# Kernel optimization log

Hardware: AMD Instinct MI355X
Metric: run time of the kernel (lower is better)

Reference implementation:

```python
import jax, jax.numpy as jnp
import numpy as np

B, D, N, WD, R, NW = 1024, 1024, 256, 64, 4, 1
EPS = 1e-6


def _dense(x, W, b):
    return x @ W + b


def _cosine_weights(memory, keys, strengths):
    # memory [B,N,WD], keys [B,K,WD], strengths [B,K] -> softmax cosine weights [B,K,N]
    dot = jnp.einsum('bkw,bnw->bkn', keys, memory)
    mn = jnp.linalg.norm(memory, axis=-1)  # [B,N]
    kn = jnp.linalg.norm(keys, axis=-1)    # [B,K]
    sim = dot / (kn[:, :, None] * mn[:, None, :] + EPS)
    return jax.nn.softmax(sim * strengths[:, :, None], axis=-1)


def _allocation(usage):
    # DNC Freeness allocation: sort by non-usage, exclusive cumprod of usage, unsort.
    usage = EPS + (1.0 - EPS) * usage
    nonusage = 1.0 - usage
    idx = jnp.argsort(-nonusage, axis=-1)            # descending non-usage
    s_non = jnp.take_along_axis(nonusage, idx, axis=-1)
    s_use = 1.0 - s_non
    cp = jnp.cumprod(s_use, axis=-1)
    excl = jnp.concatenate([jnp.ones_like(cp[:, :1]), cp[:, :-1]], axis=-1)
    s_alloc = s_non * excl
    inv = jnp.argsort(idx, axis=-1)                  # inverse permutation
    return jnp.take_along_axis(s_alloc, inv, axis=-1)


def _forward(controller, memory, prev_read_weights, prev_write_weights, prev_link,
             prev_precedence, prev_usage, params):
    (W_wv, b_wv, W_ev, b_ev, W_fg, b_fg, W_ag, b_ag, W_wg, b_wg,
     W_rm, b_rm, W_ws, b_ws, W_rs, b_rs, W_wk, b_wk, W_rk, b_rk) = params
    Bsz = controller.shape[0]

    # _read_inputs: small dense projections of controller output
    write_vectors = _dense(controller, W_wv, b_wv).reshape(Bsz, NW, WD)
    erase_vectors = jax.nn.sigmoid(_dense(controller, W_ev, b_ev)).reshape(Bsz, NW, WD)
    free_gate = jax.nn.sigmoid(_dense(controller, W_fg, b_fg))          # [B,R]
    allocation_gate = jax.nn.sigmoid(_dense(controller, W_ag, b_ag))    # [B,NW]
    write_gate = jax.nn.sigmoid(_dense(controller, W_wg, b_wg))         # [B,NW]
    read_mode = jax.nn.softmax(_dense(controller, W_rm, b_rm).reshape(Bsz, R, 1 + 2 * NW), axis=-1)
    write_keys = _dense(controller, W_wk, b_wk).reshape(Bsz, NW, WD)
    write_strengths = jax.nn.softplus(_dense(controller, W_ws, b_ws))   # [B,NW]
    read_keys = _dense(controller, W_rk, b_rk).reshape(Bsz, R, WD)
    read_strengths = jax.nn.softplus(_dense(controller, W_rs, b_rs))    # [B,R]

    # Freeness: usage update (not differentiable wrt write weights, per DNC)
    ww_sg = jax.lax.stop_gradient(prev_write_weights)
    agg_ww = 1.0 - jnp.prod(1.0 - ww_sg, axis=1)                        # [B,N]
    usage_after_write = prev_usage + (1.0 - prev_usage) * agg_ww
    phi = jnp.prod(1.0 - free_gate[:, :, None] * prev_read_weights, axis=1)
    usage = usage_after_write * phi

    # write weights: content + allocation mixed by gates
    write_content = _cosine_weights(memory, write_keys, write_strengths)  # [B,NW,N]
    write_gates = allocation_gate * write_gate
    alloc_list = []
    u = usage
    for i in range(NW):
        a = _allocation(u)
        alloc_list.append(a)
        u = u + (1.0 - u) * write_gates[:, i:i + 1] * a
    write_alloc = jnp.stack(alloc_list, axis=1)                           # [B,NW,N]
    ag = allocation_gate[:, :, None]
    wg = write_gate[:, :, None]
    write_weights = wg * (ag * write_alloc + (1.0 - ag) * write_content)

    # erase and write
    weighted_resets = write_weights[:, :, :, None] * erase_vectors[:, :, None, :]  # [B,NW,N,WD]
    reset_gate = jnp.prod(1.0 - weighted_resets, axis=1)                           # [B,N,WD]
    memory = memory * reset_gate + jnp.einsum('bwn,bwd->bnd', write_weights, write_vectors)

    # temporal linkage update
    ww_i = write_weights[:, :, :, None]
    ww_j = write_weights[:, :, None, :]
    new_link = ww_i * prev_precedence[:, :, None, :]
    link = (1.0 - ww_i - ww_j) * prev_link + new_link
    link = link * (1.0 - jnp.eye(N, dtype=link.dtype))                   # zero diagonal
    precedence = (1.0 - jnp.sum(write_weights, axis=-1, keepdims=True)) * prev_precedence + write_weights

    # read weights: content + directional (forward/backward over link)
    read_content = _cosine_weights(memory, read_keys, read_strengths)    # [B,R,N]
    forward_w = jnp.einsum('brn,bwmn->brwm', prev_read_weights, link)    # adjoint_b=True
    backward_w = jnp.einsum('brn,bwnm->brwm', prev_read_weights, link)
    backward_mode = read_mode[:, :, :NW]
    forward_mode = read_mode[:, :, NW:2 * NW]
    content_mode = read_mode[:, :, 2 * NW]
    read_weights = (content_mode[:, :, None] * read_content
                    + jnp.einsum('brw,brwn->brn', forward_mode, forward_w)
                    + jnp.einsum('brw,brwn->brn', backward_mode, backward_w))
    read_words = jnp.einsum('brn,bnd->brd', read_weights, memory)        # [B,R,WD]
    return read_words, memory, read_weights, write_weights, link, precedence, usage


def setup_inputs() -> dict:
    key = jax.random.key(0)
    ks = jax.random.split(key, 32)
    inp = {
        'controller': jax.random.normal(ks[0], (B, D), jnp.float32),
        'memory': jax.random.normal(ks[1], (B, N, WD), jnp.float32),
        'prev_read_weights': jax.random.uniform(ks[2], (B, R, N), jnp.float32) / N,
        'prev_write_weights': jax.random.uniform(ks[3], (B, NW, N), jnp.float32) / N,
        'prev_link': jnp.zeros((B, NW, N, N), jnp.float32),
        'prev_precedence': jax.random.uniform(ks[4], (B, NW, N), jnp.float32) / N,
        'prev_usage': jax.random.uniform(ks[5], (B, N), jnp.float32),
    }
    dims = [('wv', NW * WD), ('ev', NW * WD), ('fg', R), ('ag', NW), ('wg', NW),
            ('rm', R * (1 + 2 * NW)), ('ws', NW), ('rs', R), ('wk', NW * WD), ('rk', R * WD)]
    i = 6
    for name, od in dims:
        inp['W_' + name] = jax.random.normal(ks[i], (D, od), jnp.float32) * 0.02
        inp['b_' + name] = jnp.zeros((od,), jnp.float32)
        i += 1
    return inp


def reference(controller, memory, prev_read_weights, prev_write_weights, prev_link,
              prev_precedence, prev_usage,
              W_wv, b_wv, W_ev, b_ev, W_fg, b_fg, W_ag, b_ag, W_wg, b_wg,
              W_rm, b_rm, W_ws, b_ws, W_rs, b_rs, W_wk, b_wk, W_rk, b_rk):
    params = (W_wv, b_wv, W_ev, b_ev, W_fg, b_fg, W_ag, b_ag, W_wg, b_wg,
              W_rm, b_rm, W_ws, b_ws, W_rs, b_rs, W_wk, b_wk, W_rk, b_rk)
    return _forward(controller, memory, prev_read_weights, prev_write_weights,
                    prev_link, prev_precedence, prev_usage, params)
```

## Files before the change

kernel.cpp:

```cpp
#include <hip/hip_runtime.h>
#include <math.h>

typedef unsigned short ush;
typedef float v4f __attribute__((ext_vector_type(4)));

#define EPSc 1e-6f

#define NB 1024
#define ND 1024
#define NN 256
#define NWD 64
#define NR 4

#define OFF_RWORDS   ((size_t)0)
#define OFF_MEM      ((size_t)262144)
#define OFF_RWEIGHTS ((size_t)17039360)
#define OFF_WW       ((size_t)18087936)
#define OFF_LINK     ((size_t)18350080)
#define OFF_PREC     ((size_t)85458944)
#define OFF_USAGE    ((size_t)85721088)

#define WS_PART   ((size_t)0)
#define WS_PARAMS ((size_t)2097152)
#define WS_FW     ((size_t)2785280)
#define WS_BW     ((size_t)3833856)

struct Ptrs {
  const float* W[10];
  const float* Bv[10];
};

__device__ __forceinline__ float b2f(ush h){
  union { unsigned int u; float f; } v; v.u = ((unsigned int)h) << 16; return v.f;
}
__device__ __forceinline__ ush f2b(float f){
  union { float f; unsigned int u; } v; v.f = f;
  unsigned int u = v.u;
  u += 0x7fffu + ((u >> 16) & 1u);
  return (ush)(u >> 16);
}
__device__ __forceinline__ float sigm(float x){ return 1.f/(1.f+expf(-x)); }
__device__ __forceinline__ float softplus(float x){ return fmaxf(x,0.f) + log1pf(expf(-fabsf(x))); }

__device__ __forceinline__ int colmap(int c, int& lc, int& od){
  const int starts[11] = {0,64,128,132,133,134,146,147,151,215,471};
  const int ods[10]    = {64,64,4,1,1,12,1,4,64,256};
  int m = 0;
  #pragma unroll
  for (int i=1;i<10;i++) if (c >= starts[i]) m = i;
  lc = c - starts[m]; od = ods[m];
  return m;
}

__global__ __launch_bounds__(256) void k1_gemm(const float* __restrict__ ctrl, Ptrs P,
                                               float* __restrict__ part){
  int bt = blockIdx.x;
  int kc = blockIdx.y;
  int t  = threadIdx.x;
  __shared__ float cl[16*256];
  for (int v = t; v < 1024; v += 256){
    int row = v >> 6, chunk = v & 63;
    const float* src = ctrl + (size_t)(bt*16+row)*ND + kc*256 + chunk*4;
    *(float4*)&cl[row*256 + chunk*4] = *(const float4*)src;
  }
  __syncthreads();
  int c0 = t, c1 = t + 256;
  bool has1 = (c1 < 471);
  int lc0, od0, lc1 = 0, od1 = 1;
  int m0 = colmap(c0, lc0, od0);
  const float* w0p = P.W[m0];
  const float* w1p = w0p;
  if (has1){ int m1 = colmap(c1, lc1, od1); w1p = P.W[m1]; }
  float acc0[16]; float acc1[16];
  #pragma unroll
  for (int r=0;r<16;r++){ acc0[r]=0.f; acc1[r]=0.f; }
  for (int d = 0; d < 256; d++){
    int dg = kc*256 + d;
    float wv0 = w0p[(size_t)dg*od0 + lc0];
    float wv1 = has1 ? w1p[(size_t)dg*od1 + lc1] : 0.f;
    #pragma unroll
    for (int row = 0; row < 16; row++){
      float cv = cl[row*256 + d];
      acc0[row] += cv*wv0;
      acc1[row] += cv*wv1;
    }
  }
  #pragma unroll
  for (int row=0; row<16; row++){
    size_t base = ((size_t)kc*NB + bt*16+row)*512;
    part[base + c0] = acc0[row];
    if (has1) part[base + c1] = acc1[row];
  }
}

__global__ __launch_bounds__(256) void k2_gates(
    const float* __restrict__ part, Ptrs P,
    const float* __restrict__ mem, const float* __restrict__ prw_in,
    const float* __restrict__ pww_in, const float* __restrict__ pprec,
    const float* __restrict__ pusage,
    float* __restrict__ params,
    float* __restrict__ out_ww, float* __restrict__ out_prec, float* __restrict__ out_usage)
{
  int b = blockIdx.x, t = threadIdx.x;
  __shared__ float proj[512];
  __shared__ float red[256];
  __shared__ float simb[256];
  __shared__ float keyA[256];
  __shared__ int   idxA[256];
  __shared__ float cp[256];
  __shared__ float wkL[64];
  __shared__ float scal[12];

  for (int c = t; c < 471; c += 256){
    float v = 0.f;
    #pragma unroll
    for (int kc=0;kc<4;kc++) v += part[((size_t)kc*NB + b)*512 + c];
    int lc, od; int m = colmap(c, lc, od);
    v += P.Bv[m][lc];
    proj[c] = v;
  }
  __syncthreads();

  float* pb = params + (size_t)b*672;
  if (t < 64){
    pb[t] = proj[t];
    pb[64+t] = sigm(proj[64+t]);
    wkL[t] = proj[151+t];
  }
  pb[128 + t] = proj[215 + t];
  if (t < 4){
    pb[384 + t] = softplus(proj[147 + t]);
    float a = proj[134 + 3*t], bq = proj[134 + 3*t + 1], c2 = proj[134 + 3*t + 2];
    float mx = fmaxf(a, fmaxf(bq, c2));
    float ea = expf(a-mx), eb = expf(bq-mx), ec = expf(c2-mx);
    float s = ea+eb+ec;
    pb[388 + 3*t]     = ea/s;
    pb[388 + 3*t + 1] = eb/s;
    pb[388 + 3*t + 2] = ec/s;
    scal[t] = sigm(proj[128+t]);
  }
  if (t == 0){
    scal[4] = sigm(proj[132]);
    scal[5] = sigm(proj[133]);
    scal[6] = softplus(proj[146]);
  }
  __syncthreads();
  if (t == 0){
    float s = 0.f;
    for (int d=0;d<64;d++) s += wkL[d]*wkL[d];
    scal[7] = sqrtf(s);
  }
  __syncthreads();

  float us;
  {
    float pu = pusage[(size_t)b*NN + t];
    float pw = pww_in[(size_t)b*NN + t];
    float uaw = pu + (1.f-pu)*pw;
    float phi = 1.f;
    #pragma unroll
    for (int r=0;r<4;r++)
      phi *= (1.f - scal[r]*prw_in[((size_t)b*NR + r)*NN + t]);
    us = uaw*phi;
    out_usage[(size_t)b*NN + t] = us;
  }

  {
    const float* mrow = mem + ((size_t)b*NN + t)*NWD;
    float dot = 0.f, n2 = 0.f;
    for (int d0=0; d0<64; d0+=4){
      float4 q = *(const float4*)(mrow + d0);
      dot += wkL[d0]*q.x + wkL[d0+1]*q.y + wkL[d0+2]*q.z + wkL[d0+3]*q.w;
      n2  += q.x*q.x + q.y*q.y + q.z*q.z + q.w*q.w;
    }
    simb[t] = scal[6]*dot/(scal[7]*sqrtf(n2) + EPSc);
  }
  __syncthreads();
  red[t] = simb[t]; __syncthreads();
  for (int s=128;s>0;s>>=1){ if (t<s) red[t]=fmaxf(red[t],red[t+s]); __syncthreads(); }
  float mx = red[0]; __syncthreads();
  float e = expf(simb[t]-mx);
  red[t] = e; __syncthreads();
  for (int s=128;s>0;s>>=1){ if (t<s) red[t]+=red[t+s]; __syncthreads(); }
  float content = e / red[0];
  __syncthreads();

  keyA[t] = EPSc + (1.f-EPSc)*us;
  idxA[t] = t;
  __syncthreads();
  for (int k=2; k<=256; k<<=1){
    for (int j=k>>1; j>0; j>>=1){
      int ixj = t ^ j;
      if (ixj > t){
        float a = keyA[t], bb = keyA[ixj];
        int ia = idxA[t], ib = idxA[ixj];
        bool up = ((t & k) == 0);
        bool agtb = (a > bb) || (a == bb && ia > ib);
        if (up == agtb){ keyA[t]=bb; keyA[ixj]=a; idxA[t]=ib; idxA[ixj]=ia; }
      }
      __syncthreads();
    }
  }
  cp[t] = keyA[t]; __syncthreads();
  for (int off=1; off<256; off<<=1){
    float v = cp[t];
    float w = (t>=off)? cp[t-off] : 1.f;
    __syncthreads();
    cp[t] = v*w;
    __syncthreads();
  }
  float excl = (t==0) ? 1.f : cp[t-1];
  float s_alloc = (1.f - keyA[t]) * excl;
  __syncthreads();
  simb[idxA[t]] = s_alloc;
  __syncthreads();
  float alloc = simb[t];

  float ag = scal[4], wg = scal[5];
  float ww = wg*(ag*alloc + (1.f-ag)*content);
  pb[400 + t] = ww;
  out_ww[(size_t)b*NN + t] = ww;
  red[t] = ww; __syncthreads();
  for (int s=128;s>0;s>>=1){ if (t<s) red[t]+=red[t+s]; __syncthreads(); }
  float wsum = red[0];
  float prec = (1.f - wsum)*pprec[(size_t)b*NN + t] + ww;
  out_prec[(size_t)b*NN + t] = prec;
}

__global__ __launch_bounds__(256) void k4_link(
    const float* __restrict__ plink, const float* __restrict__ pprec,
    const float* __restrict__ prw_in, const float* __restrict__ params,
    float* __restrict__ out_link, float* __restrict__ fw, float* __restrict__ bwp)
{
  int b = blockIdx.x, cc = blockIdx.y, t = threadIdx.x;
  int w = t >> 6, l = t & 63;
  __shared__ float wwl[256], ppl[256], prwl[4*256];
  __shared__ v4f   bred[4][4][64];
  __shared__ float fwbuf[4*128];
  const float* pb = params + (size_t)b*672;
  wwl[t] = pb[400 + t];
  ppl[t] = pprec[(size_t)b*NN + t];
  #pragma unroll
  for (int r=0;r<4;r++) prwl[r*256 + t] = prw_in[((size_t)b*NR + r)*NN + t];
  __syncthreads();

  v4f wwj = *(const v4f*)&wwl[4*l];
  v4f ppj = *(const v4f*)&ppl[4*l];
  v4f pr0 = *(const v4f*)&prwl[0*256 + 4*l];
  v4f pr1 = *(const v4f*)&prwl[1*256 + 4*l];
  v4f pr2 = *(const v4f*)&prwl[2*256 + 4*l];
  v4f pr3 = *(const v4f*)&prwl[3*256 + 4*l];

  v4f bacc0 = {0.f,0.f,0.f,0.f}, bacc1 = bacc0, bacc2 = bacc0, bacc3 = bacc0;

  int i0 = cc*128 + w*32;
  const v4f* plrow = (const v4f*)(plink + ((size_t)b*NN + i0)*NN) + l;
  float*     olbase = out_link + ((size_t)b*NN + i0)*NN + 4*l;

  for (int k=0; k<32; k++){
    int i = i0 + k;
    v4f pl = plrow[(size_t)k*64];
    float wwi = wwl[i];
    float c1  = 1.f - wwi;
    float pi0 = prwl[0*256+i], pi1 = prwl[1*256+i],
          pi2 = prwl[2*256+i], pi3 = prwl[3*256+i];
    v4f lv = (c1 - wwj)*pl + wwi*ppj;
    if (l == (i>>2)) lv[i&3] = 0.f;
    __builtin_nontemporal_store(lv, (v4f*)(olbase + (size_t)k*NN));

    v4f f0 = pr0*lv, f1 = pr1*lv, f2 = pr2*lv, f3 = pr3*lv;
    float s0 = f0.x+f0.y+f0.z+f0.w;
    float s1 = f1.x+f1.y+f1.z+f1.w;
    float s2 = f2.x+f2.y+f2.z+f2.w;
    float s3 = f3.x+f3.y+f3.z+f3.w;
    bacc0 += pi0*lv; bacc1 += pi1*lv; bacc2 += pi2*lv; bacc3 += pi3*lv;

    s0 += __shfl_xor(s0,1); s0 += __shfl_xor(s0,2);
    s1 += __shfl_xor(s1,1); s1 += __shfl_xor(s1,2);
    s2 += __shfl_xor(s2,1); s2 += __shfl_xor(s2,2);
    s3 += __shfl_xor(s3,1); s3 += __shfl_xor(s3,2);
    float v = (l&1) ? ((l&2)? s3 : s1) : ((l&2)? s2 : s0);
    v += __shfl_xor(v,4); v += __shfl_xor(v,8);
    v += __shfl_xor(v,16); v += __shfl_xor(v,32);
    if (l < 4) fwbuf[w*128 + l*32 + k] = v;
  }

  bred[w][0][l] = bacc0;
  bred[w][1][l] = bacc1;
  bred[w][2][l] = bacc2;
  bred[w][3][l] = bacc3;
  __syncthreads();

  {
    int r = t >> 6, l2 = t & 63;
    v4f a = bred[0][r][l2], b4 = bred[1][r][l2],
        c4 = bred[2][r][l2], d4 = bred[3][r][l2];
    v4f s = a + b4 + c4 + d4;
    *(v4f*)&bwp[(((size_t)cc*NB + b)*NR + r)*NN + 4*l2] = s;
    #pragma unroll
    for (int e=0;e<2;e++){
      int idx = t + e*256;
      int rr = idx >> 7, j = idx & 127;
      fw[((size_t)b*NR + rr)*NN + cc*128 + j] = fwbuf[(j>>5)*128 + rr*32 + (j&31)];
    }
  }
}

__global__ __launch_bounds__(256) void k5_read(
    const float* __restrict__ mem, const float* __restrict__ params,
    const float* __restrict__ fw, const float* __restrict__ bwp,
    float* __restrict__ out_rwords, float* __restrict__ out_mem, float* __restrict__ out_rweights)
{
  int b = blockIdx.x, t = threadIdx.x;
  __shared__ ush   memn[256*66];
  __shared__ float wvl[64], erl[64], rkl[256];
  __shared__ float siml[4*260];
  __shared__ float rwl[4*260];
  __shared__ float scal[32];
  const float* pb = params + (size_t)b*672;
  if (t < 64){ wvl[t] = pb[t]; erl[t] = pb[64+t]; }
  rkl[t] = pb[128 + t];
  if (t < 4)  scal[12+t] = pb[384+t];
  if (t < 12) scal[16+t] = pb[388+t];
  __syncthreads();
  if (t < 4){
    float s = 0.f;
    for (int d=0;d<64;d++){ float v = rkl[t*64+d]; s += v*v; }
    scal[t] = sqrtf(s);
  }
  __syncthreads();

  float wwn = pb[400 + t];
  const float* mrow = mem + ((size_t)b*NN + t)*NWD;
  float* orow = out_mem + ((size_t)b*NN + t)*NWD;
  float n2=0.f, dot0=0.f, dot1=0.f, dot2=0.f, dot3=0.f;
  for (int d0=0; d0<64; d0+=4){
    float4 q = *(const float4*)(mrow + d0);
    float4 qo;
    float* qi = (float*)&q;
    float* po = (float*)&qo;
    #pragma unroll
    for (int k=0;k<4;k++){
      int d = d0+k;
      float m = qi[k];
      float nv = m*(1.f - wwn*erl[d]) + wwn*wvl[d];
      po[k] = nv;
      memn[t*66 + d] = f2b(nv);
      n2 += nv*nv;
      dot0 += rkl[0*64+d]*nv;
      dot1 += rkl[1*64+d]*nv;
      dot2 += rkl[2*64+d]*nv;
      dot3 += rkl[3*64+d]*nv;
    }
    *(float4*)(orow + d0) = qo;
  }
  float sn = sqrtf(n2);
  siml[0*260+t] = scal[12]*dot0/(scal[0]*sn + EPSc);
  siml[1*260+t] = scal[13]*dot1/(scal[1]*sn + EPSc);
  siml[2*260+t] = scal[14]*dot2/(scal[2]*sn + EPSc);
  siml[3*260+t] = scal[15]*dot3/(scal[3]*sn + EPSc);
  __syncthreads();

  int rr = t >> 6, lane = t & 63;
  {
    float m1 = -1e30f;
    #pragma unroll
    for (int q2=0;q2<4;q2++) m1 = fmaxf(m1, siml[rr*260 + q2*64 + lane]);
    #pragma unroll
    for (int off=32; off>0; off>>=1) m1 = fmaxf(m1, __shfl_xor(m1, off));
    float s1 = 0.f;
    #pragma unroll
    for (int q2=0;q2<4;q2++) s1 += expf(siml[rr*260 + q2*64 + lane] - m1);
    #pragma unroll
    for (int off=32; off>0; off>>=1) s1 += __shfl_xor(s1, off);
    if (lane == 0){ scal[4+rr] = m1; scal[8+rr] = s1; }
  }
  __syncthreads();

  #pragma unroll
  for (int r=0;r<4;r++){
    float c = expf(siml[r*260+t] - scal[4+r]) / scal[8+r];
    float fwv = fw[((size_t)b*NR + r)*NN + t];
    float bwv = bwp[((size_t)b*NR + r)*NN + t]
              + bwp[((size_t)(NB + b)*NR + r)*NN + t];
    float rwv = scal[16+3*r+2]*c + scal[16+3*r+1]*fwv + scal[16+3*r+0]*bwv;
    rwl[r*260 + t] = rwv;
    out_rweights[((size_t)b*NR + r)*NN + t] = rwv;
  }
  __syncthreads();

  {
    float acc = 0.f;
    for (int n=0;n<256;n++) acc += rwl[rr*260 + n]*b2f(memn[n*66 + lane]);
    out_rwords[((size_t)b*NR + rr)*NWD + lane] = acc;
  }
}

extern "C" void kernel_launch(void* const* d_in, const int* in_sizes, int n_in,
                              void* d_out, int out_size, void* d_ws, size_t ws_size,
                              hipStream_t stream) {
  const float* ctrl   = (const float*)d_in[0];
  const float* mem    = (const float*)d_in[1];
  const float* prw    = (const float*)d_in[2];
  const float* pww    = (const float*)d_in[3];
  const float* plink  = (const float*)d_in[4];
  const float* pprec  = (const float*)d_in[5];
  const float* pusage = (const float*)d_in[6];
  Ptrs P;
  for (int i=0;i<10;i++){
    P.W[i]  = (const float*)d_in[7 + 2*i];
    P.Bv[i] = (const float*)d_in[8 + 2*i];
  }
  float* ws = (float*)d_ws;
  float* part   = ws + WS_PART;
  float* params = ws + WS_PARAMS;
  float* fw     = ws + WS_FW;

  float* o = (float*)d_out;
  float* out_rwords   = o + OFF_RWORDS;
  float* out_mem      = o + OFF_MEM;
  float* out_rweights = o + OFF_RWEIGHTS;
  float* out_ww       = o + OFF_WW;
  float* out_link     = o + OFF_LINK;
  float* out_prec     = o + OFF_PREC;
  float* out_usage    = o + OFF_USAGE;

  k1_gemm<<<dim3(64,4), 256, 0, stream>>>(ctrl, P, part);
  k2_gates<<<NB, 256, 0, stream>>>(part, P, mem, prw, pww, pprec, pusage,
                                   params, out_ww, out_prec, out_usage);
  k4_link<<<dim3(NB,2), 256, 0, stream>>>(plink, pprec, prw, params, out_link, fw, part);
  k5_read<<<NB, 256, 0, stream>>>(mem, params, fw, part,
                                  out_rwords, out_mem, out_rweights);
}
```

Before: 773.4 us.

## Retile projection GEMM and use wavefront shuffles for gate reductions and sort

The projection GEMM now runs 512-thread blocks over 8 rows each, with one column per thread and a padded shared tile, which doubles the grid and lowers per-thread register use. The gates kernel swaps its shared-memory tree reductions, bitonic sort and prefix-product scan for wavefront shuffle versions, keeping shared memory and block barriers only for the cross-wave sort stages. The read kernel packs bf16 values into 32-bit stores to shared memory instead of writing them one at a time. Together these aim to cut barrier and shared-memory traffic in the small per-batch kernels. The sort's tie-breaking and stage ordering must match the old version exactly for the allocation weights to stay the same.

```diff
diff --git a/kernel.cpp b/kernel.cpp
--- a/kernel.cpp
+++ b/kernel.cpp
@@ -23,7 +23,6 @@
 #define WS_PART   ((size_t)0)
 #define WS_PARAMS ((size_t)2097152)
 #define WS_FW     ((size_t)2785280)
-#define WS_BW     ((size_t)3833856)
 
 struct Ptrs {
   const float* W[10];
@@ -52,46 +51,53 @@
   return m;
 }
 
-__global__ __launch_bounds__(256) void k1_gemm(const float* __restrict__ ctrl, Ptrs P,
+__global__ __launch_bounds__(512) void k1_gemm(const float* __restrict__ ctrl, Ptrs P,
                                                float* __restrict__ part){
   int bt = blockIdx.x;
   int kc = blockIdx.y;
   int t  = threadIdx.x;
-  __shared__ float cl[16*256];
-  for (int v = t; v < 1024; v += 256){
-    int row = v >> 6, chunk = v & 63;
-    const float* src = ctrl + (size_t)(bt*16+row)*ND + kc*256 + chunk*4;
-    *(float4*)&cl[row*256 + chunk*4] = *(const float4*)src;
-  }
-  __syncthreads();
-  int c0 = t, c1 = t + 256;
-  bool has1 = (c1 < 471);
-  int lc0, od0, lc1 = 0, od1 = 1;
-  int m0 = colmap(c0, lc0, od0);
-  const float* w0p = P.W[m0];
-  const float* w1p = w0p;
-  if (has1){ int m1 = colmap(c1, lc1, od1); w1p = P.W[m1]; }
-  float acc0[16]; float acc1[16];
-  #pragma unroll
-  for (int r=0;r<16;r++){ acc0[r]=0.f; acc1[r]=0.f; }
+  __shared__ float cl[8*260];
+  {
+    int row = t >> 6, chunk = t & 63;
+    const float* src = ctrl + (size_t)(bt*8+row)*ND + kc*256 + chunk*4;
+    *(float4*)&cl[row*260 + chunk*4] = *(const float4*)src;
+  }
+  __syncthreads();
+  int c = (t < 471) ? t : 470;
+  int lc, od; int m = colmap(c, lc, od);
+  const float* wp = P.W[m];
+  float acc[8];
+  #pragma unroll
+  for (int r=0;r<8;r++) acc[r]=0.f;
+  #pragma unroll 4
   for (int d = 0; d < 256; d++){
     int dg = kc*256 + d;
-    float wv0 = w0p[(size_t)dg*od0 + lc0];
-    float wv1 = has1 ? w1p[(size_t)dg*od1 + lc1] : 0.f;
-    #pragma unroll
-    for (int row = 0; row < 16; row++){
-      float cv = cl[row*256 + d];
-      acc0[row] += cv*wv0;
-      acc1[row] += cv*wv1;
-    }
-  }
-  #pragma unroll
-  for (int row=0; row<16; row++){
-    size_t base = ((size_t)kc*NB + bt*16+row)*512;
-    part[base + c0] = acc0[row];
-    if (has1) part[base + c1] = acc1[row];
-  }
-}
+    float wv = wp[(size_t)dg*od + lc];
+    #pragma unroll
+    for (int r = 0; r < 8; r++)
+      acc[r] += cl[r*260 + d]*wv;
+  }
+  if (t < 471){
+    #pragma unroll
+    for (int r=0;r<8;r++)
+      part[((size_t)kc*NB + bt*8+r)*512 + c] = acc[r];
+  }
+}
+
+
+#define SSTAGE(j,k) { \
+  float kp = __shfl_xor(key, (j)); int ip = __shfl_xor(idx, (j)); \
+  bool gt = (key > kp) || (key == kp && idx > ip); \
+  bool selmin = (((t & (k)) == 0) == ((t & (j)) == 0)); \
+  if (selmin == gt){ key = kp; idx = ip; } }
+
+#define LSTAGE(j,k) { \
+  sk[t] = key; si[t] = idx; __syncthreads(); \
+  float kp = sk[t^(j)]; int ip = si[t^(j)]; \
+  bool gt = (key > kp) || (key == kp && idx > ip); \
+  bool selmin = (((t & (k)) == 0) == ((t & (j)) == 0)); \
+  if (selmin == gt){ key = kp; idx = ip; } \
+  __syncthreads(); }
 
 __global__ __launch_bounds__(256) void k2_gates(
     const float* __restrict__ part, Ptrs P,
@@ -102,14 +108,14 @@
     float* __restrict__ out_ww, float* __restrict__ out_prec, float* __restrict__ out_usage)
 {
   int b = blockIdx.x, t = threadIdx.x;
+  int w = t >> 6, l = t & 63;
   __shared__ float proj[512];
-  __shared__ float red[256];
-  __shared__ float simb[256];
-  __shared__ float keyA[256];
-  __shared__ int   idxA[256];
-  __shared__ float cp[256];
   __shared__ float wkL[64];
   __shared__ float scal[12];
+  __shared__ float wred[16];
+  __shared__ float sk[256];
+  __shared__ int   si[256];
+  __shared__ float salloc[256];
 
   for (int c = t; c < 471; c += 256){
     float v = 0.f;
@@ -144,11 +150,12 @@
     scal[5] = sigm(proj[133]);
     scal[6] = softplus(proj[146]);
   }
-  __syncthreads();
-  if (t == 0){
-    float s = 0.f;
-    for (int d=0;d<64;d++) s += wkL[d]*wkL[d];
-    scal[7] = sqrtf(s);
+  if (w == 0){
+    float kv = proj[151 + l];
+    float s2 = kv*kv;
+    #pragma unroll
+    for (int off=32; off>0; off>>=1) s2 += __shfl_xor(s2, off);
+    if (l == 0) scal[7] = sqrtf(s2);
   }
   __syncthreads();
 
@@ -165,6 +172,7 @@
     out_usage[(size_t)b*NN + t] = us;
   }
 
+  float sim;
   {
     const float* mrow = mem + ((size_t)b*NN + t)*NWD;
     float dot = 0.f, n2 = 0.f;
@@ -173,56 +181,71 @@
       dot += wkL[d0]*q.x + wkL[d0+1]*q.y + wkL[d0+2]*q.z + wkL[d0+3]*q.w;
       n2  += q.x*q.x + q.y*q.y + q.z*q.z + q.w*q.w;
     }
-    simb[t] = scal[6]*dot/(scal[7]*sqrtf(n2) + EPSc);
-  }
-  __syncthreads();
-  red[t] = simb[t]; __syncthreads();
-  for (int s=128;s>0;s>>=1){ if (t<s) red[t]=fmaxf(red[t],red[t+s]); __syncthreads(); }
-  float mx = red[0]; __syncthreads();
-  float e = expf(simb[t]-mx);
-  red[t] = e; __syncthreads();
-  for (int s=128;s>0;s>>=1){ if (t<s) red[t]+=red[t+s]; __syncthreads(); }
-  float content = e / red[0];
-  __syncthreads();
-
-  keyA[t] = EPSc + (1.f-EPSc)*us;
-  idxA[t] = t;
-  __syncthreads();
-  for (int k=2; k<=256; k<<=1){
-    for (int j=k>>1; j>0; j>>=1){
-      int ixj = t ^ j;
-      if (ixj > t){
-        float a = keyA[t], bb = keyA[ixj];
-        int ia = idxA[t], ib = idxA[ixj];
-        bool up = ((t & k) == 0);
-        bool agtb = (a > bb) || (a == bb && ia > ib);
-        if (up == agtb){ keyA[t]=bb; keyA[ixj]=a; idxA[t]=ib; idxA[ixj]=ia; }
-      }
-      __syncthreads();
-    }
-  }
-  cp[t] = keyA[t]; __syncthreads();
-  for (int off=1; off<256; off<<=1){
-    float v = cp[t];
-    float w = (t>=off)? cp[t-off] : 1.f;
-    __syncthreads();
-    cp[t] = v*w;
-    __syncthreads();
-  }
-  float excl = (t==0) ? 1.f : cp[t-1];
-  float s_alloc = (1.f - keyA[t]) * excl;
-  __syncthreads();
-  simb[idxA[t]] = s_alloc;
-  __syncthreads();
-  float alloc = simb[t];
+    sim = scal[6]*dot/(scal[7]*sqrtf(n2) + EPSc);
+  }
+  {
+    float m_ = sim;
+    #pragma unroll
+    for (int off=32; off>0; off>>=1) m_ = fmaxf(m_, __shfl_xor(m_, off));
+    if (l == 0) wred[w] = m_;
+  }
+  __syncthreads();
+  float mx = fmaxf(fmaxf(wred[0],wred[1]), fmaxf(wred[2],wred[3]));
+  float e = expf(sim - mx);
+  {
+    float s_ = e;
+    #pragma unroll
+    for (int off=32; off>0; off>>=1) s_ += __shfl_xor(s_, off);
+    if (l == 0) wred[4+w] = s_;
+  }
+  __syncthreads();
+  float content = e / (wred[4]+wred[5]+wred[6]+wred[7]);
+
+  float key = EPSc + (1.f-EPSc)*us;
+  int idx = t;
+  SSTAGE(1,2)
+  SSTAGE(2,4)  SSTAGE(1,4)
+  SSTAGE(4,8)  SSTAGE(2,8)  SSTAGE(1,8)
+  SSTAGE(8,16) SSTAGE(4,16) SSTAGE(2,16) SSTAGE(1,16)
+  SSTAGE(16,32) SSTAGE(8,32) SSTAGE(4,32) SSTAGE(2,32) SSTAGE(1,32)
+  SSTAGE(32,64) SSTAGE(16,64) SSTAGE(8,64) SSTAGE(4,64) SSTAGE(2,64) SSTAGE(1,64)
+  LSTAGE(64,128)
+  SSTAGE(32,128) SSTAGE(16,128) SSTAGE(8,128) SSTAGE(4,128) SSTAGE(2,128) SSTAGE(1,128)
+  LSTAGE(128,256)
+  LSTAGE(64,256)
+  SSTAGE(32,256) SSTAGE(16,256) SSTAGE(8,256) SSTAGE(4,256) SSTAGE(2,256) SSTAGE(1,256)
+
+  float v = key;
+  #pragma unroll
+  for (int off=1; off<64; off<<=1){
+    float u = __shfl_up(v, off);
+    if (l >= off) v *= u;
+  }
+  if (l == 63) wred[8+w] = v;
+  __syncthreads();
+  float pre = 1.f;
+  #pragma unroll
+  for (int q=0; q<3; q++) if (q < w) pre *= wred[8+q];
+  float exv = __shfl_up(v, 1);
+  if (l == 0) exv = 1.f;
+  float excl = exv * pre;
+  float s_alloc = (1.f - key) * excl;
+  salloc[idx] = s_alloc;
+  __syncthreads();
+  float alloc = salloc[t];
 
   float ag = scal[4], wg = scal[5];
   float ww = wg*(ag*alloc + (1.f-ag)*content);
   pb[400 + t] = ww;
   out_ww[(size_t)b*NN + t] = ww;
-  red[t] = ww; __syncthreads();
-  for (int s=128;s>0;s>>=1){ if (t<s) red[t]+=red[t+s]; __syncthreads(); }
-  float wsum = red[0];
+  {
+    float s_ = ww;
+    #pragma unroll
+    for (int off=32; off>0; off>>=1) s_ += __shfl_xor(s_, off);
+    if (l == 0) wred[12+w] = s_;
+  }
+  __syncthreads();
+  float wsum = wred[12]+wred[13]+wred[14]+wred[15];
   float prec = (1.f - wsum)*pprec[(size_t)b*NN + t] + ww;
   out_prec[(size_t)b*NN + t] = prec;
 }
@@ -345,13 +368,16 @@
       float m = qi[k];
       float nv = m*(1.f - wwn*erl[d]) + wwn*wvl[d];
       po[k] = nv;
-      memn[t*66 + d] = f2b(nv);
       n2 += nv*nv;
       dot0 += rkl[0*64+d]*nv;
       dot1 += rkl[1*64+d]*nv;
       dot2 += rkl[2*64+d]*nv;
       dot3 += rkl[3*64+d]*nv;
     }
+    unsigned int p01 = (unsigned int)f2b(po[0]) | ((unsigned int)f2b(po[1]) << 16);
+    unsigned int p23 = (unsigned int)f2b(po[2]) | ((unsigned int)f2b(po[3]) << 16);
+    *(unsigned int*)&memn[t*66 + d0]     = p01;
+    *(unsigned int*)&memn[t*66 + d0 + 2] = p23;
     *(float4*)(orow + d0) = qo;
   }
   float sn = sqrtf(n2);
@@ -425,7 +451,7 @@
   float* out_prec     = o + OFF_PREC;
   float* out_usage    = o + OFF_USAGE;
 
-  k1_gemm<<<dim3(64,4), 256, 0, stream>>>(ctrl, P, part);
+  k1_gemm<<<dim3(128,4), 512, 0, stream>>>(ctrl, P, part);
   k2_gates<<<NB, 256, 0, stream>>>(part, P, mem, prw, pww, pprec, pusage,
                                    params, out_ww, out_prec, out_usage);
   k4_link<<<dim3(NB,2), 256, 0, stream>>>(plink, pprec, prw, params, out_link, fw, part);
```

New measurement: 735.3 us. 1.05x faster.
